# Kernel optimization log

Measured on AMD Instinct MI355X. Metric: run time of the kernel, lower is better.

## Reference

```python
import jax, jax.numpy as jnp
import numpy as np

N_EXPERTS = 256
TOP_K = 8
N_GROUPS = 8
N_LIMITED = 4
EXPERTS_PER_GROUP = N_EXPERTS // N_GROUPS
ROUTE_SCALE = 2.5


def setup_inputs() -> dict:
    key = jax.random.key(0)
    k1, k2, k3 = jax.random.split(key, 3)
    T, D = 16384, 2048
    x = jax.random.normal(k1, (T, D), dtype=jnp.float32)
    # kaiming_uniform-ish scale for the router weight
    bound = 1.0 / np.sqrt(D)
    weight = jax.random.uniform(k2, (N_EXPERTS, D), dtype=jnp.float32, minval=-bound, maxval=bound)
    expert_bias = 0.01 * jax.random.normal(k3, (N_EXPERTS,), dtype=jnp.float32)
    return {"x": x, "weight": weight, "expert_bias": expert_bias}


def reference(x, weight, expert_bias):
    T = x.shape[0]
    # router logits -> softmax scores  [T, E]
    scores = jax.nn.softmax(jnp.einsum("td,ed->te", x, weight), axis=-1)
    # training path: bias-adjusted scores used only for selection
    sel = scores + expert_bias[None, :]
    # group-limited routing: keep only top n_limited groups per token
    group_scores = sel.reshape(T, N_GROUPS, EXPERTS_PER_GROUP).max(axis=-1)  # [T, G]
    _, top_groups = jax.lax.top_k(group_scores, N_LIMITED)  # [T, n_limited]
    group_mask = jnp.any(jax.nn.one_hot(top_groups, N_GROUPS, dtype=jnp.bool_), axis=1)  # [T, G]
    expert_mask = jnp.repeat(group_mask, EXPERTS_PER_GROUP, axis=-1)  # [T, E]
    sel = jnp.where(expert_mask, sel, -jnp.inf)
    # top-k experts per token (indices from bias-adjusted/masked scores)
    _, topk_indices = jax.lax.top_k(sel, TOP_K)  # [T, k]
    # gating weights gathered from the ORIGINAL softmax scores
    weights = jnp.take_along_axis(scores, topk_indices, axis=-1) * ROUTE_SCALE  # [T, k]
    # expert load tracking (scatter_add over flattened indices)
    load = jax.ops.segment_sum(
        jnp.ones((T * TOP_K,), dtype=jnp.float32),
        topk_indices.reshape(-1),
        num_segments=N_EXPERTS,
    )
    return weights, topk_indices, load
```

## Files before the change

### kernel.cpp

```cpp
#include <hip/hip_runtime.h>
#include <hip/hip_fp16.h>
#include <math.h>

#define T_TOKENS 16384
#define D_DIM    2048
#define NEXP     256
#define TOPK     8
#define NLIM     4
#define BM       32
#define NSS      16
#define NTHREADS 512

typedef __attribute__((ext_vector_type(8))) _Float16 f16x8;
typedef __attribute__((ext_vector_type(4))) float f32x4;

struct GemmBufs { unsigned short A[2][4][2][64][8]; };
union SMem {
  GemmBufs g;
  float Sc[BM][260];
};

__global__ __launch_bounds__(256) void prep_w(const float* __restrict__ w,
                                              unsigned short* __restrict__ wf) {
  const int g   = blockIdx.x * 256 + threadIdx.x;
  const int kc  = g >> 10;
  const int rem = g & 1023;
  const int nfg = rem >> 6;
  const int l   = rem & 63;
  const int e   = nfg * 16 + (l & 15);
  const int kb  = kc * 32 + ((l >> 4) << 3);
  const float* src = &w[(size_t)e * D_DIM + kb];
  float f[8];
  *reinterpret_cast<float4*>(&f[0]) = *reinterpret_cast<const float4*>(src);
  *reinterpret_cast<float4*>(&f[4]) = *reinterpret_cast<const float4*>(src + 4);
  union { unsigned short s[8]; float4 v; } h;
  #pragma unroll
  for (int j = 0; j < 8; ++j) h.s[j] = __half_as_ushort(__float2half(f[j]));
  *reinterpret_cast<float4*>(wf + (size_t)kc * 8192 + nfg * 512 + l * 8) = h.v;
}

__device__ __forceinline__ unsigned cvt2(float a, float b) {
  return (unsigned)__half_as_ushort(__float2half(a)) |
         ((unsigned)__half_as_ushort(__float2half(b)) << 16);
}
__device__ __forceinline__ uint4 pack8(const float4& lo, const float4& hi) {
  uint4 p;
  p.x = cvt2(lo.x, lo.y); p.y = cvt2(lo.z, lo.w);
  p.z = cvt2(hi.x, hi.y); p.w = cvt2(hi.z, hi.w);
  return p;
}

__device__ __forceinline__ void body(
    int n, const float* asrc, const unsigned short* wfB,
    int ksw, int mfw, int lnw, int lane,
    float4& xc0, float4& xc1,
    float4& xn0, float4& xn1,
    SMem& sm, f32x4 (&acc)[2][2]) {
  if (n + 2 < NSS) {
    const float* s = asrc + (size_t)(n + 2) * 128;
    xn0 = *reinterpret_cast<const float4*>(s);
    xn1 = *reinterpret_cast<const float4*>(s + 4);
  }
  __builtin_amdgcn_sched_barrier(0);
  f16x8 b[2][4];
  #pragma unroll
  for (int nf = 0; nf < 2; ++nf)
    #pragma unroll
    for (int ks = 0; ks < 4; ++ks)
      b[nf][ks] = *reinterpret_cast<const f16x8*>(
          wfB + (size_t)(n * 4 + ks) * 8192 + nf * 512);
  const int ring = n & 1;
  f16x8 a[2][4];
  #pragma unroll
  for (int mf = 0; mf < 2; ++mf)
    #pragma unroll
    for (int ks = 0; ks < 4; ++ks)
      a[mf][ks] = *reinterpret_cast<const f16x8*>(&sm.g.A[ring][ks][mf][lane][0]);
  #pragma unroll
  for (int ks = 0; ks < 4; ++ks)
    #pragma unroll
    for (int mf = 0; mf < 2; ++mf) {
      acc[mf][0] = __builtin_amdgcn_mfma_f32_16x16x32_f16(a[mf][ks], b[0][ks], acc[mf][0], 0, 0, 0);
      acc[mf][1] = __builtin_amdgcn_mfma_f32_16x16x32_f16(a[mf][ks], b[1][ks], acc[mf][1], 0, 0, 0);
    }
  __builtin_amdgcn_sched_barrier(0);
  if (n + 1 < NSS) {
    uint4 p = pack8(xc0, xc1);
    *reinterpret_cast<uint4*>(&sm.g.A[ring ^ 1][ksw][mfw][lnw][0]) = p;
  }
  asm volatile("s_waitcnt lgkmcnt(0)" ::: "memory");
  __builtin_amdgcn_sched_barrier(0);
  __builtin_amdgcn_s_barrier();
  __builtin_amdgcn_sched_barrier(0);
}

__global__ __launch_bounds__(NTHREADS, 4) void gate_kernel(
    const float* __restrict__ x,
    const unsigned short* __restrict__ wf,
    const float* __restrict__ bias,
    float* __restrict__ out_w,
    float* __restrict__ out_idx,
    float* __restrict__ out_load) {

  __shared__ SMem sm;
  __shared__ int hist[NEXP];

  const int tid  = threadIdx.x;
  const int row0 = blockIdx.x * BM;
  const int lane = tid & 63;
  const int wid  = tid >> 6;

  for (int i = tid; i < NEXP; i += NTHREADS) hist[i] = 0;

  const int ksw = tid >> 7;
  const int mfw = (tid >> 6) & 1;
  const int lnw = tid & 63;
  const float* asrc = &x[(size_t)(row0 + mfw * 16 + (lnw & 15)) * D_DIM +
                         ksw * 32 + ((lnw >> 4) << 3)];
  const unsigned short* wfB = wf + (size_t)(wid * 2) * 512 + (size_t)lane * 8;

  f32x4 acc[2][2];
  #pragma unroll
  for (int i = 0; i < 2; ++i)
    #pragma unroll
    for (int j = 0; j < 2; ++j) acc[i][j] = (f32x4)(0.0f);

  float4 xA0, xA1, xB0, xB1;
  {
    float4 p0 = *reinterpret_cast<const float4*>(asrc);
    float4 p1 = *reinterpret_cast<const float4*>(asrc + 4);
    xA0 = *reinterpret_cast<const float4*>(asrc + 128);
    xA1 = *reinterpret_cast<const float4*>(asrc + 132);
    uint4 p = pack8(p0, p1);
    *reinterpret_cast<uint4*>(&sm.g.A[0][ksw][mfw][lnw][0]) = p;
  }
  asm volatile("s_waitcnt lgkmcnt(0)" ::: "memory");
  __builtin_amdgcn_sched_barrier(0);
  __builtin_amdgcn_s_barrier();
  __builtin_amdgcn_sched_barrier(0);

  for (int n = 0; n < NSS; n += 2) {
    body(n,     asrc, wfB, ksw, mfw, lnw, lane, xA0, xA1, xB0, xB1, sm, acc);
    body(n + 1, asrc, wfB, ksw, mfw, lnw, lane, xB0, xB1, xA0, xA1, sm, acc);
  }
  __syncthreads();

  #pragma unroll
  for (int mf = 0; mf < 2; ++mf)
    #pragma unroll
    for (int nf = 0; nf < 2; ++nf)
      #pragma unroll
      for (int r = 0; r < 4; ++r) {
        const int row = mf * 16 + ((lane >> 4) << 2) + r;
        const int col = wid * 32 + nf * 16 + (lane & 15);
        sm.Sc[row][col] = acc[mf][nf][r];
      }
  __syncthreads();

  const float4 bsl = *reinterpret_cast<const float4*>(&bias[lane * 4]);
  const int g = lane >> 3;

  for (int m = wid; m < BM; m += 8) {
    float v[4];
    *reinterpret_cast<float4*>(v) =
        *reinterpret_cast<const float4*>(&sm.Sc[m][lane * 4]);

    float mx = fmaxf(fmaxf(v[0], v[1]), fmaxf(v[2], v[3]));
    #pragma unroll
    for (int s = 1; s < 64; s <<= 1) mx = fmaxf(mx, __shfl_xor(mx, s));
    float ex[4], sum = 0.f;
    #pragma unroll
    for (int j = 0; j < 4; ++j) { ex[j] = expf(v[j] - mx); sum += ex[j]; }
    #pragma unroll
    for (int s = 1; s < 64; s <<= 1) sum += __shfl_xor(sum, s);
    float sc[4], sel[4];
    sc[0] = ex[0] / sum; sc[1] = ex[1] / sum;
    sc[2] = ex[2] / sum; sc[3] = ex[3] / sum;
    sel[0] = sc[0] + bsl.x; sel[1] = sc[1] + bsl.y;
    sel[2] = sc[2] + bsl.z; sel[3] = sc[3] + bsl.w;

    *reinterpret_cast<float4*>(&sm.Sc[m][lane * 4]) =
        make_float4(sc[0], sc[1], sc[2], sc[3]);

    float gv = fmaxf(fmaxf(sel[0], sel[1]), fmaxf(sel[2], sel[3]));
    gv = fmaxf(gv, __shfl_xor(gv, 1));
    gv = fmaxf(gv, __shfl_xor(gv, 2));
    gv = fmaxf(gv, __shfl_xor(gv, 4));

    unsigned gmask = 0;
    float gcur = gv;
    #pragma unroll
    for (int it = 0; it < NLIM; ++it) {
      float bv2 = gcur; int bi = g;
      #pragma unroll
      for (int s = 1; s < 64; s <<= 1) {
        float ov = __shfl_xor(bv2, s);
        int   oi = __shfl_xor(bi, s);
        if (ov > bv2 || (ov == bv2 && oi < bi)) { bv2 = ov; bi = oi; }
      }
      gmask |= 1u << bi;
      if (g == bi) gcur = -INFINITY;
    }
    if (!((gmask >> g) & 1u)) {
      sel[0] = sel[1] = sel[2] = sel[3] = -INFINITY;
    }

    const int gtok = row0 + m;
    #pragma unroll
    for (int it = 0; it < TOPK; ++it) {
      float bv2 = sel[0]; int bi = lane * 4;
      #pragma unroll
      for (int j = 1; j < 4; ++j)
        if (sel[j] > bv2) { bv2 = sel[j]; bi = lane * 4 + j; }
      #pragma unroll
      for (int s = 1; s < 64; s <<= 1) {
        float ov = __shfl_xor(bv2, s);
        int   oi = __shfl_xor(bi, s);
        if (ov > bv2 || (ov == bv2 && oi < bi)) { bv2 = ov; bi = oi; }
      }
      if (lane == 0) {
        out_w[(size_t)gtok * TOPK + it]   = sm.Sc[m][bi] * 2.5f;
        out_idx[(size_t)gtok * TOPK + it] = (float)bi;
        atomicAdd(&hist[bi], 1);
      }
      if ((bi >> 2) == lane) sel[bi & 3] = -INFINITY;
    }
  }

  __syncthreads();
  for (int b = tid; b < NEXP; b += NTHREADS)
    if (hist[b]) atomicAdd(&out_load[b], (float)hist[b]);
}

extern "C" void kernel_launch(void* const* d_in, const int* in_sizes, int n_in,
                              void* d_out, int out_size, void* d_ws, size_t ws_size,
                              hipStream_t stream) {
  const float* x    = (const float*)d_in[0];
  const float* w    = (const float*)d_in[1];
  const float* bias = (const float*)d_in[2];
  float* out_w    = (float*)d_out;
  float* out_idx  = out_w + (size_t)T_TOKENS * TOPK;
  float* out_load = out_idx + (size_t)T_TOKENS * TOPK;
  unsigned short* wfrag = (unsigned short*)d_ws;

  (void)hipMemsetAsync(out_load, 0, NEXP * sizeof(float), stream);
  prep_w<<<256, 256, 0, stream>>>(w, wfrag);
  gate_kernel<<<T_TOKENS / BM, NTHREADS, 0, stream>>>(
      x, wfrag, bias, out_w, out_idx, out_load);
}
```

Baseline: 105.6 us.

## Prefetch next-stage weight fragments into registers and restructure routing epilogue per token

The GEMM loop now loads the B (weight) fragments for step n+1 into a second register set while the MFMAs for step n run, double-buffering B in registers. The A fragments are read from LDS per k-slice and used right away. The routing epilogue is reorganized so that each group of 8 lanes handles one token, and each lane holds a full 32-expert group in registers. Only 4 waves do the epilogue, and the reductions need only 3 shuffle steps instead of 6. The price is much higher register pressure (B buffers plus 64 floats per lane in the epilogue), which may reduce occupancy or cause spills.

Result: faster. 87.07 us (-17.5%).

```diff
diff --git a/kernel.cpp b/kernel.cpp
--- a/kernel.cpp
+++ b/kernel.cpp
@@ -50,39 +50,41 @@
   return p;
 }
 
+__device__ __forceinline__ void loadB(f16x8 (&b)[2][4], int n,
+                                      const unsigned short* wfB) {
+  #pragma unroll
+  for (int nf = 0; nf < 2; ++nf)
+    #pragma unroll
+    for (int ks = 0; ks < 4; ++ks)
+      b[nf][ks] = *reinterpret_cast<const f16x8*>(
+          wfB + (size_t)(n * 4 + ks) * 8192 + nf * 512);
+}
+
 __device__ __forceinline__ void body(
     int n, const float* asrc, const unsigned short* wfB,
     int ksw, int mfw, int lnw, int lane,
     float4& xc0, float4& xc1,
     float4& xn0, float4& xn1,
+    f16x8 (&bc)[2][4],
+    f16x8 (&bn)[2][4],
     SMem& sm, f32x4 (&acc)[2][2]) {
   if (n + 2 < NSS) {
     const float* s = asrc + (size_t)(n + 2) * 128;
     xn0 = *reinterpret_cast<const float4*>(s);
     xn1 = *reinterpret_cast<const float4*>(s + 4);
   }
-  __builtin_amdgcn_sched_barrier(0);
-  f16x8 b[2][4];
-  #pragma unroll
-  for (int nf = 0; nf < 2; ++nf)
-    #pragma unroll
-    for (int ks = 0; ks < 4; ++ks)
-      b[nf][ks] = *reinterpret_cast<const f16x8*>(
-          wfB + (size_t)(n * 4 + ks) * 8192 + nf * 512);
+  if (n + 1 < NSS) loadB(bn, n + 1, wfB);
+  __builtin_amdgcn_sched_barrier(0);
   const int ring = n & 1;
-  f16x8 a[2][4];
-  #pragma unroll
-  for (int mf = 0; mf < 2; ++mf)
-    #pragma unroll
-    for (int ks = 0; ks < 4; ++ks)
-      a[mf][ks] = *reinterpret_cast<const f16x8*>(&sm.g.A[ring][ks][mf][lane][0]);
-  #pragma unroll
-  for (int ks = 0; ks < 4; ++ks)
-    #pragma unroll
-    for (int mf = 0; mf < 2; ++mf) {
-      acc[mf][0] = __builtin_amdgcn_mfma_f32_16x16x32_f16(a[mf][ks], b[0][ks], acc[mf][0], 0, 0, 0);
-      acc[mf][1] = __builtin_amdgcn_mfma_f32_16x16x32_f16(a[mf][ks], b[1][ks], acc[mf][1], 0, 0, 0);
-    }
+  #pragma unroll
+  for (int ks = 0; ks < 4; ++ks) {
+    f16x8 a0 = *reinterpret_cast<const f16x8*>(&sm.g.A[ring][ks][0][lane][0]);
+    f16x8 a1 = *reinterpret_cast<const f16x8*>(&sm.g.A[ring][ks][1][lane][0]);
+    acc[0][0] = __builtin_amdgcn_mfma_f32_16x16x32_f16(a0, bc[0][ks], acc[0][0], 0, 0, 0);
+    acc[0][1] = __builtin_amdgcn_mfma_f32_16x16x32_f16(a0, bc[1][ks], acc[0][1], 0, 0, 0);
+    acc[1][0] = __builtin_amdgcn_mfma_f32_16x16x32_f16(a1, bc[0][ks], acc[1][0], 0, 0, 0);
+    acc[1][1] = __builtin_amdgcn_mfma_f32_16x16x32_f16(a1, bc[1][ks], acc[1][1], 0, 0, 0);
+  }
   __builtin_amdgcn_sched_barrier(0);
   if (n + 1 < NSS) {
     uint4 p = pack8(xc0, xc1);
@@ -126,11 +128,13 @@
     for (int j = 0; j < 2; ++j) acc[i][j] = (f32x4)(0.0f);
 
   float4 xA0, xA1, xB0, xB1;
+  f16x8 bA[2][4], bB[2][4];
   {
     float4 p0 = *reinterpret_cast<const float4*>(asrc);
     float4 p1 = *reinterpret_cast<const float4*>(asrc + 4);
     xA0 = *reinterpret_cast<const float4*>(asrc + 128);
     xA1 = *reinterpret_cast<const float4*>(asrc + 132);
+    loadB(bA, 0, wfB);
     uint4 p = pack8(p0, p1);
     *reinterpret_cast<uint4*>(&sm.g.A[0][ksw][mfw][lnw][0]) = p;
   }
@@ -140,8 +144,8 @@
   __builtin_amdgcn_sched_barrier(0);
 
   for (int n = 0; n < NSS; n += 2) {
-    body(n,     asrc, wfB, ksw, mfw, lnw, lane, xA0, xA1, xB0, xB1, sm, acc);
-    body(n + 1, asrc, wfB, ksw, mfw, lnw, lane, xB0, xB1, xA0, xA1, sm, acc);
+    body(n,     asrc, wfB, ksw, mfw, lnw, lane, xA0, xA1, xB0, xB1, bA, bB, sm, acc);
+    body(n + 1, asrc, wfB, ksw, mfw, lnw, lane, xB0, xB1, xA0, xA1, bB, bA, sm, acc);
   }
   __syncthreads();
 
@@ -157,73 +161,92 @@
       }
   __syncthreads();
 
-  const float4 bsl = *reinterpret_cast<const float4*>(&bias[lane * 4]);
-  const int g = lane >> 3;
-
-  for (int m = wid; m < BM; m += 8) {
-    float v[4];
-    *reinterpret_cast<float4*>(v) =
-        *reinterpret_cast<const float4*>(&sm.Sc[m][lane * 4]);
-
-    float mx = fmaxf(fmaxf(v[0], v[1]), fmaxf(v[2], v[3]));
-    #pragma unroll
-    for (int s = 1; s < 64; s <<= 1) mx = fmaxf(mx, __shfl_xor(mx, s));
-    float ex[4], sum = 0.f;
-    #pragma unroll
-    for (int j = 0; j < 4; ++j) { ex[j] = expf(v[j] - mx); sum += ex[j]; }
-    #pragma unroll
-    for (int s = 1; s < 64; s <<= 1) sum += __shfl_xor(sum, s);
-    float sc[4], sel[4];
-    sc[0] = ex[0] / sum; sc[1] = ex[1] / sum;
-    sc[2] = ex[2] / sum; sc[3] = ex[3] / sum;
-    sel[0] = sc[0] + bsl.x; sel[1] = sc[1] + bsl.y;
-    sel[2] = sc[2] + bsl.z; sel[3] = sc[3] + bsl.w;
-
-    *reinterpret_cast<float4*>(&sm.Sc[m][lane * 4]) =
-        make_float4(sc[0], sc[1], sc[2], sc[3]);
-
-    float gv = fmaxf(fmaxf(sel[0], sel[1]), fmaxf(sel[2], sel[3]));
-    gv = fmaxf(gv, __shfl_xor(gv, 1));
-    gv = fmaxf(gv, __shfl_xor(gv, 2));
-    gv = fmaxf(gv, __shfl_xor(gv, 4));
-
-    unsigned gmask = 0;
+  if (wid < 4) {
+    const int t8  = lane >> 3;
+    const int g2  = lane & 7;
+    const int tokl = wid * 8 + t8;
+    const int gtok = row0 + tokl;
+
+    float sc[32], sel[32];
+    #pragma unroll
+    for (int jc = 0; jc < 8; ++jc) {
+      const int c = (jc + g2) & 7;
+      float4 v = *reinterpret_cast<const float4*>(&sm.Sc[tokl][g2 * 32 + c * 4]);
+      sc[jc * 4 + 0] = v.x; sc[jc * 4 + 1] = v.y;
+      sc[jc * 4 + 2] = v.z; sc[jc * 4 + 3] = v.w;
+    }
+    float mx = sc[0];
+    #pragma unroll
+    for (int s = 1; s < 32; ++s) mx = fmaxf(mx, sc[s]);
+    mx = fmaxf(mx, __shfl_xor(mx, 1));
+    mx = fmaxf(mx, __shfl_xor(mx, 2));
+    mx = fmaxf(mx, __shfl_xor(mx, 4));
+    float sum = 0.f;
+    #pragma unroll
+    for (int s = 0; s < 32; ++s) { sc[s] = expf(sc[s] - mx); sum += sc[s]; }
+    sum += __shfl_xor(sum, 1);
+    sum += __shfl_xor(sum, 2);
+    sum += __shfl_xor(sum, 4);
+    #pragma unroll
+    for (int s = 0; s < 32; ++s) sc[s] = sc[s] / sum;
+    #pragma unroll
+    for (int jc = 0; jc < 8; ++jc) {
+      const int c = (jc + g2) & 7;
+      float4 b4 = *reinterpret_cast<const float4*>(&bias[g2 * 32 + c * 4]);
+      sel[jc * 4 + 0] = sc[jc * 4 + 0] + b4.x;
+      sel[jc * 4 + 1] = sc[jc * 4 + 1] + b4.y;
+      sel[jc * 4 + 2] = sc[jc * 4 + 2] + b4.z;
+      sel[jc * 4 + 3] = sc[jc * 4 + 3] + b4.w;
+    }
+    float gv = sel[0];
+    #pragma unroll
+    for (int s = 1; s < 32; ++s) gv = fmaxf(gv, sel[s]);
     float gcur = gv;
+    int kept = 0;
     #pragma unroll
     for (int it = 0; it < NLIM; ++it) {
-      float bv2 = gcur; int bi = g;
-      #pragma unroll
-      for (int s = 1; s < 64; s <<= 1) {
-        float ov = __shfl_xor(bv2, s);
-        int   oi = __shfl_xor(bi, s);
-        if (ov > bv2 || (ov == bv2 && oi < bi)) { bv2 = ov; bi = oi; }
-      }
-      gmask |= 1u << bi;
-      if (g == bi) gcur = -INFINITY;
-    }
-    if (!((gmask >> g) & 1u)) {
-      sel[0] = sel[1] = sel[2] = sel[3] = -INFINITY;
-    }
-
-    const int gtok = row0 + m;
+      float bv = gcur; int bl = g2;
+      #pragma unroll
+      for (int s = 1; s < 8; s <<= 1) {
+        float ov = __shfl_xor(bv, s);
+        int   ol = __shfl_xor(bl, s);
+        if (ov > bv || (ov == bv && ol < bl)) { bv = ov; bl = ol; }
+      }
+      if (g2 == bl) { kept = 1; gcur = -INFINITY; }
+    }
+    if (!kept) {
+      #pragma unroll
+      for (int s = 0; s < 32; ++s) sel[s] = -INFINITY;
+    }
     #pragma unroll
     for (int it = 0; it < TOPK; ++it) {
-      float bv2 = sel[0]; int bi = lane * 4;
-      #pragma unroll
-      for (int j = 1; j < 4; ++j)
-        if (sel[j] > bv2) { bv2 = sel[j]; bi = lane * 4 + j; }
-      #pragma unroll
-      for (int s = 1; s < 64; s <<= 1) {
-        float ov = __shfl_xor(bv2, s);
-        int   oi = __shfl_xor(bi, s);
-        if (ov > bv2 || (ov == bv2 && oi < bi)) { bv2 = ov; bi = oi; }
-      }
-      if (lane == 0) {
-        out_w[(size_t)gtok * TOPK + it]   = sm.Sc[m][bi] * 2.5f;
-        out_idx[(size_t)gtok * TOPK + it] = (float)bi;
-        atomicAdd(&hist[bi], 1);
-      }
-      if ((bi >> 2) == lane) sel[bi & 3] = -INFINITY;
+      float lv = -INFINITY; int lei = 0x7FFFFFFF, lslot = -1;
+      #pragma unroll
+      for (int s = 0; s < 32; ++s) {
+        const int eidx = g2 * 32 + (((s >> 2) + g2) & 7) * 4 + (s & 3);
+        if (sel[s] > lv || (sel[s] == lv && eidx < lei)) {
+          lv = sel[s]; lei = eidx; lslot = s;
+        }
+      }
+      float bv = lv; int bei = lei;
+      #pragma unroll
+      for (int s = 1; s < 8; s <<= 1) {
+        float ov = __shfl_xor(bv, s);
+        int   oe = __shfl_xor(bei, s);
+        if (ov > bv || (ov == bv && oe < bei)) { bv = ov; bei = oe; }
+      }
+      const bool win = ((bei >> 5) == g2);
+      if (win) {
+        float wv = 0.f;
+        #pragma unroll
+        for (int s = 0; s < 32; ++s) if (s == lslot) wv = sc[s];
+        out_w[(size_t)gtok * TOPK + it]   = wv * 2.5f;
+        out_idx[(size_t)gtok * TOPK + it] = (float)bei;
+        atomicAdd(&hist[bei], 1);
+      }
+      #pragma unroll
+      for (int s = 0; s < 32; ++s)
+        if (win && s == lslot) sel[s] = -INFINITY;
     }
   }
 
```
